# Optimization experiments

Measured on AMD Instinct MI355X. Metric: run time of the kernel, lower is better.

Reference implementation:

```python
import jax, jax.numpy as jnp
import numpy as np

P, LMAX, D, H = 4096, 64, 512, 512
NEG = -1e30


def setup_inputs() -> dict:
    key = jax.random.key(0)
    ks = jax.random.split(key, 8)
    paths_nodes = jax.random.normal(ks[0], (P, LMAX, D), dtype=jnp.float32)
    lengths = jax.random.randint(ks[1], (P,), 1, LMAX + 1, dtype=jnp.int32)
    s = 0.05
    return {
        "paths_nodes": paths_nodes,
        "lengths": lengths,
        "pW1": jax.random.normal(ks[2], (D, H), dtype=jnp.float32) * s,
        "pb1": jnp.zeros((H,), dtype=jnp.float32),
        "pw2": jax.random.normal(ks[3], (H,), dtype=jnp.float32) * s,
        "pb2": jnp.zeros((1,), dtype=jnp.float32),
        "aW1": jax.random.normal(ks[4], (D, H), dtype=jnp.float32) * s,
        "ab1": jnp.zeros((H,), dtype=jnp.float32),
        "aw2": jax.random.normal(ks[5], (H,), dtype=jnp.float32) * s,
        "ab2": jnp.zeros((1,), dtype=jnp.float32),
    }


def reference(paths_nodes, lengths, pW1, pb1, pw2, pb2, aW1, ab1, aw2, ab2):
    # paths_nodes: [P, L, D], lengths: [P]
    mask = jnp.arange(LMAX)[None, :] < lengths[:, None]  # [P, L] valid positions

    # per-path node attention: Linear -> ReLU -> Linear(->1), softmax over length
    h = jax.nn.relu(jnp.einsum('pld,dh->plh', paths_nodes, pW1) + pb1)  # [P,L,H]
    scores = jnp.einsum('plh,h->pl', h, pw2) + pb2[0]                   # [P,L]
    scores = jnp.where(mask, scores, NEG)
    w = jax.nn.softmax(scores, axis=1)                                  # [P,L]
    paths_fea = jnp.einsum('pl,pld->pd', w, paths_nodes)                # [P,D]

    # path-level attention: same MLP over path features, softmax over paths
    h2 = jax.nn.relu(paths_fea @ aW1 + ab1)                             # [P,H]
    a = h2 @ aw2 + ab2[0]                                               # [P]
    aw = jax.nn.softmax(a, axis=0)                                      # [P]
    user_fea = jnp.einsum('p,pd->d', aw, paths_fea)                     # [D]
    return user_fea
```

## Files before the change

kernel.cpp:

```cpp
#include <hip/hip_runtime.h>

typedef __attribute__((ext_vector_type(8))) short bf16x8;
typedef __attribute__((ext_vector_type(8))) unsigned short u16x8;
typedef __attribute__((ext_vector_type(4))) float f32x4;

__device__ __forceinline__ ushort f2bf(float x) {
  unsigned u = __float_as_uint(x);
  unsigned r = (u + 0x7fffu + ((u >> 16) & 1u)) >> 16;
  return (ushort)r;
}

__global__ void transpose_convert(const float* __restrict__ w1, const float* __restrict__ w2,
                                  ushort* __restrict__ o1, ushort* __restrict__ o2) {
  __shared__ float tile[64][65];
  const float* src = (blockIdx.z == 0) ? w1 : w2;
  ushort* dst = (blockIdx.z == 0) ? o1 : o2;
  const int n0 = blockIdx.x * 64, k0 = blockIdx.y * 64;
  const int tx = threadIdx.x, ty = threadIdx.y;
#pragma unroll
  for (int i = 0; i < 16; ++i) {
    int k = ty + i * 4;
    tile[k][tx] = src[(size_t)(k0 + k) * 512 + n0 + tx];
  }
  __syncthreads();
#pragma unroll
  for (int i = 0; i < 16; ++i) {
    int n = ty + i * 4;
    dst[(size_t)(n0 + n) * 512 + k0 + tx] = f2bf(tile[tx][n]);
  }
}

__launch_bounds__(256, 3)
__global__ void gemm_score(const float* __restrict__ A,
                           const ushort* __restrict__ Bt,
                           const float* __restrict__ bias,
                           const float* __restrict__ wout,
                           float* __restrict__ scores) {
  __shared__ ushort As[128 * 64];
  __shared__ ushort Bs[128 * 64];
  __shared__ float sred[2][128];
  const int tid = threadIdx.x;
  const int wv = tid >> 6, lane = tid & 63;
  const int ln = lane & 15, quad = lane >> 4;
  const int wm = wv & 1, wn = wv >> 1;
  const int m0 = blockIdx.y * 128;
  const int nb = blockIdx.x * 128;

  float bv[4], w2v[4];
#pragma unroll
  for (int ns = 0; ns < 4; ++ns) {
    int n = nb + wn * 64 + ns * 16 + ln;
    bv[ns] = bias[n];
    w2v[ns] = wout[n];
  }

  f32x4 acc[4][4];
  const f32x4 zero = {0.f, 0.f, 0.f, 0.f};
#pragma unroll
  for (int i = 0; i < 4; ++i)
#pragma unroll
    for (int j = 0; j < 4; ++j) acc[i][j] = zero;

  int arow[4], brow[4];
#pragma unroll
  for (int ms = 0; ms < 4; ++ms) arow[ms] = wm * 64 + ms * 16 + ln;
#pragma unroll
  for (int ns = 0; ns < 4; ++ns) brow[ns] = wn * 64 + ns * 16 + ln;

  for (int kc = 0; kc < 8; ++kc) {
    const int kb = kc * 64;
    __syncthreads();
#pragma unroll
    for (int j = 0; j < 4; ++j) {
      int id = j * 256 + tid;
      int row = id >> 3, c = id & 7;
      int cs = (c ^ (row & 7)) * 8;
      const float* srcA = A + (size_t)(m0 + row) * 512 + kb + c * 8;
      float4 v0 = *(const float4*)srcA;
      float4 v1 = *(const float4*)(srcA + 4);
      u16x8 ua = {f2bf(v0.x), f2bf(v0.y), f2bf(v0.z), f2bf(v0.w),
                  f2bf(v1.x), f2bf(v1.y), f2bf(v1.z), f2bf(v1.w)};
      *(u16x8*)(&As[row * 64 + cs]) = ua;
      u16x8 ub = *(const u16x8*)(Bt + (size_t)(nb + row) * 512 + kb + c * 8);
      *(u16x8*)(&Bs[row * 64 + cs]) = ub;
    }
    __syncthreads();
#pragma unroll
    for (int k0 = 0; k0 < 2; ++k0) {
      bf16x8 af[4], bfr[4];
#pragma unroll
      for (int ms = 0; ms < 4; ++ms) {
        int r = arow[ms];
        af[ms] = *(const bf16x8*)(&As[r * 64 + (((quad + k0 * 4) ^ (r & 7)) * 8)]);
      }
#pragma unroll
      for (int ns = 0; ns < 4; ++ns) {
        int r = brow[ns];
        bfr[ns] = *(const bf16x8*)(&Bs[r * 64 + (((quad + k0 * 4) ^ (r & 7)) * 8)]);
      }
#pragma unroll
      for (int ms = 0; ms < 4; ++ms)
#pragma unroll
        for (int ns = 0; ns < 4; ++ns)
          acc[ms][ns] = __builtin_amdgcn_mfma_f32_16x16x32_bf16(af[ms], bfr[ns], acc[ms][ns], 0, 0, 0);
    }
  }

#pragma unroll
  for (int ms = 0; ms < 4; ++ms) {
#pragma unroll
    for (int r = 0; r < 4; ++r) {
      float s = 0.f;
#pragma unroll
      for (int ns = 0; ns < 4; ++ns)
        s += fmaxf(acc[ms][ns][r] + bv[ns], 0.f) * w2v[ns];
      s += __shfl_xor(s, 1);
      s += __shfl_xor(s, 2);
      s += __shfl_xor(s, 4);
      s += __shfl_xor(s, 8);
      if (ln == 0) sred[wn][wm * 64 + ms * 16 + quad * 4 + r] = s;
    }
  }
  __syncthreads();
  if (tid < 128) atomicAdd(&scores[m0 + tid], sred[0][tid] + sred[1][tid]);
}

__global__ void node_softmax(float* __restrict__ s_wl, const int* __restrict__ lengths) {
  const int p = blockIdx.x * 4 + (threadIdx.x >> 6);
  const int l = threadIdx.x & 63;
  float s = s_wl[(size_t)p * 64 + l];
  const int len = lengths[p];
  const bool valid = l < len;
  float sv = valid ? s : -1e30f;
  float mx = sv;
  mx = fmaxf(mx, __shfl_xor(mx, 1));
  mx = fmaxf(mx, __shfl_xor(mx, 2));
  mx = fmaxf(mx, __shfl_xor(mx, 4));
  mx = fmaxf(mx, __shfl_xor(mx, 8));
  mx = fmaxf(mx, __shfl_xor(mx, 16));
  mx = fmaxf(mx, __shfl_xor(mx, 32));
  float e = valid ? __expf(sv - mx) : 0.f;
  float tot = e;
  tot += __shfl_xor(tot, 1);
  tot += __shfl_xor(tot, 2);
  tot += __shfl_xor(tot, 4);
  tot += __shfl_xor(tot, 8);
  tot += __shfl_xor(tot, 16);
  tot += __shfl_xor(tot, 32);
  s_wl[(size_t)p * 64 + l] = e / tot;
}

__global__ void wsum(const float* __restrict__ X, const float* __restrict__ wl,
                     float* __restrict__ fea) {
  __shared__ float w[64];
  const int p = blockIdx.x, tid = threadIdx.x;
  if (tid < 64) w[tid] = wl[(size_t)p * 64 + tid];
  __syncthreads();
  const float* Xp = X + (size_t)p * 32768;
  const int d0 = tid * 4;
  float4 a = {0.f, 0.f, 0.f, 0.f};
#pragma unroll
  for (int l = 0; l < 64; ++l) {
    float4 x = *(const float4*)(Xp + l * 512 + d0);
    a.x = fmaf(w[l], x.x, a.x);
    a.y = fmaf(w[l], x.y, a.y);
    a.z = fmaf(w[l], x.z, a.z);
    a.w = fmaf(w[l], x.w, a.w);
  }
  *(float4*)(fea + (size_t)p * 512 + d0) = a;
}

__global__ void softmax_p(const float* __restrict__ a, float* __restrict__ aw) {
  const int tid = threadIdx.x;
  const int wv = tid >> 6;
  __shared__ float redm[4];
  __shared__ float reds[4];
  float v[16];
#pragma unroll
  for (int i = 0; i < 16; ++i) v[i] = a[i * 256 + tid];
  float mx = v[0];
#pragma unroll
  for (int i = 1; i < 16; ++i) mx = fmaxf(mx, v[i]);
  mx = fmaxf(mx, __shfl_xor(mx, 1));
  mx = fmaxf(mx, __shfl_xor(mx, 2));
  mx = fmaxf(mx, __shfl_xor(mx, 4));
  mx = fmaxf(mx, __shfl_xor(mx, 8));
  mx = fmaxf(mx, __shfl_xor(mx, 16));
  mx = fmaxf(mx, __shfl_xor(mx, 32));
  if ((tid & 63) == 0) redm[wv] = mx;
  __syncthreads();
  mx = fmaxf(fmaxf(redm[0], redm[1]), fmaxf(redm[2], redm[3]));
  float s = 0.f;
#pragma unroll
  for (int i = 0; i < 16; ++i) {
    v[i] = __expf(v[i] - mx);
    s += v[i];
  }
  s += __shfl_xor(s, 1);
  s += __shfl_xor(s, 2);
  s += __shfl_xor(s, 4);
  s += __shfl_xor(s, 8);
  s += __shfl_xor(s, 16);
  s += __shfl_xor(s, 32);
  if ((tid & 63) == 0) reds[wv] = s;
  __syncthreads();
  s = reds[0] + reds[1] + reds[2] + reds[3];
  const float inv = 1.f / s;
#pragma unroll
  for (int i = 0; i < 16; ++i) aw[i * 256 + tid] = v[i] * inv;
}

__global__ void user_accum(const float* __restrict__ fea, const float* __restrict__ aw,
                           float* __restrict__ out) {
  const int g = blockIdx.x, tid = threadIdx.x;
  const int d0 = tid * 2;
  float ax = 0.f, ay = 0.f;
  for (int p = g * 64; p < g * 64 + 64; ++p) {
    float w = aw[p];
    float2 x = *(const float2*)(fea + (size_t)p * 512 + d0);
    ax = fmaf(w, x.x, ax);
    ay = fmaf(w, x.y, ay);
  }
  atomicAdd(out + d0, ax);
  atomicAdd(out + d0 + 1, ay);
}

extern "C" void kernel_launch(void* const* d_in, const int* in_sizes, int n_in,
                              void* d_out, int out_size, void* d_ws, size_t ws_size,
                              hipStream_t stream) {
  const float* paths   = (const float*)d_in[0];
  const int*   lengths = (const int*)d_in[1];
  const float* pW1     = (const float*)d_in[2];
  const float* pb1     = (const float*)d_in[3];
  const float* pw2     = (const float*)d_in[4];
  const float* aW1     = (const float*)d_in[6];
  const float* ab1     = (const float*)d_in[7];
  const float* aw2     = (const float*)d_in[8];
  float* out = (float*)d_out;

  char* ws = (char*)d_ws;
  ushort* W1T  = (ushort*)ws;
  ushort* aW1T = (ushort*)(ws + 524288);
  float* nsc   = (float*)(ws + 1048576);
  float* fea   = (float*)(ws + 2097152);
  float* psc   = (float*)(ws + 10485760);
  float* awp   = (float*)(ws + 10502144);

  hipMemsetAsync(nsc, 0, 262144 * sizeof(float), stream);
  hipMemsetAsync(psc, 0, 4096 * sizeof(float), stream);
  hipMemsetAsync(d_out, 0, 512 * sizeof(float), stream);

  transpose_convert<<<dim3(8, 8, 2), dim3(64, 4), 0, stream>>>(pW1, aW1, W1T, aW1T);
  gemm_score<<<dim3(4, 2048), 256, 0, stream>>>(paths, W1T, pb1, pw2, nsc);
  node_softmax<<<1024, 256, 0, stream>>>(nsc, lengths);
  wsum<<<4096, 128, 0, stream>>>(paths, nsc, fea);
  gemm_score<<<dim3(4, 32), 256, 0, stream>>>(fea, aW1T, ab1, aw2, psc);
  softmax_p<<<1, 256, 0, stream>>>(psc, awp);
  user_accum<<<64, 256, 0, stream>>>(fea, awp, out);
}
```

Measured before the change: 985.9 us.

## Pre-convert valid path rows to bf16, skip padded rows in GEMM and weighted sum

```diff
diff --git a/kernel.cpp b/kernel.cpp
--- a/kernel.cpp
+++ b/kernel.cpp
@@ -8,6 +8,12 @@
   unsigned u = __float_as_uint(x);
   unsigned r = (u + 0x7fffu + ((u >> 16) & 1u)) >> 16;
   return (ushort)r;
+}
+
+typedef const __attribute__((address_space(1))) unsigned int ga_uint;
+typedef __attribute__((address_space(3))) unsigned int lds_uint;
+__device__ __forceinline__ void gload_lds16(const ushort* g, ushort* l) {
+  __builtin_amdgcn_global_load_lds((ga_uint*)g, (lds_uint*)l, 16, 0, 0);
 }
 
 __global__ void transpose_convert(const float* __restrict__ w1, const float* __restrict__ w2,
@@ -30,12 +36,120 @@
   }
 }
 
+__global__ void convert_x(const float* __restrict__ X, const int* __restrict__ lengths,
+                          ushort* __restrict__ Y) {
+  const int stride = gridDim.x * blockDim.x;
+  for (int i = blockIdx.x * blockDim.x + threadIdx.x; i < 16777216; i += stride) {
+    const int row = i >> 6;
+    const int l = row & 63, p = row >> 6;
+    if (l < lengths[p]) {
+      const float* s = X + (size_t)i * 8;
+      float4 v0 = *(const float4*)s;
+      float4 v1 = *(const float4*)(s + 4);
+      u16x8 o = {f2bf(v0.x), f2bf(v0.y), f2bf(v0.z), f2bf(v0.w),
+                 f2bf(v1.x), f2bf(v1.y), f2bf(v1.z), f2bf(v1.w)};
+      *(u16x8*)(Y + (size_t)i * 8) = o;
+    }
+  }
+}
+
 __launch_bounds__(256, 3)
-__global__ void gemm_score(const float* __restrict__ A,
-                           const ushort* __restrict__ Bt,
-                           const float* __restrict__ bias,
-                           const float* __restrict__ wout,
-                           float* __restrict__ scores) {
+__global__ void gemm_score_bf16(const ushort* __restrict__ A,
+                                const ushort* __restrict__ Bt,
+                                const float* __restrict__ bias,
+                                const float* __restrict__ wout,
+                                const int* __restrict__ lengths,
+                                float* __restrict__ scores) {
+  __shared__ ushort As[128 * 64] __attribute__((aligned(16)));
+  __shared__ ushort Bs[128 * 64] __attribute__((aligned(16)));
+  __shared__ float sred[2][128];
+  const int tid = threadIdx.x;
+  const int wv = tid >> 6, lane = tid & 63;
+  const int ln = lane & 15, quad = lane >> 4;
+  const int wm = wv & 1, wn = wv >> 1;
+  const int m0 = blockIdx.y * 128;
+  const int nb = blockIdx.x * 128;
+  const int p0 = m0 >> 6;
+
+  const int len0 = lengths[p0], len1 = lengths[p0 + 1];
+  const int mylen = wm ? len1 : len0;
+  const int nms = (mylen + 15) >> 4;
+
+  float bv[4], w2v[4];
+#pragma unroll
+  for (int ns = 0; ns < 4; ++ns) {
+    int n = nb + wn * 64 + ns * 16 + ln;
+    bv[ns] = bias[n];
+    w2v[ns] = wout[n];
+  }
+
+  f32x4 acc[4][4];
+  const f32x4 zero = {0.f, 0.f, 0.f, 0.f};
+#pragma unroll
+  for (int i = 0; i < 4; ++i)
+#pragma unroll
+    for (int j = 0; j < 4; ++j) acc[i][j] = zero;
+
+  for (int kc = 0; kc < 8; ++kc) {
+    const int kb = kc * 64;
+    __syncthreads();
+#pragma unroll
+    for (int i = 0; i < 4; ++i) {
+      const int id = i * 256 + tid;
+      const int row = id >> 3, c = id & 7;
+      const int base = (i * 256 + (tid & ~63)) * 8;
+      const int r0 = i * 32 + wv * 8;
+      const int rlen = (r0 < 64) ? len0 : len1;
+      if ((r0 & 63) < rlen)
+        gload_lds16(A + (size_t)(m0 + row) * 512 + kb + c * 8, &As[base]);
+      gload_lds16(Bt + (size_t)(nb + row) * 512 + kb + c * 8, &Bs[base]);
+    }
+    __syncthreads();
+#pragma unroll
+    for (int k0 = 0; k0 < 2; ++k0) {
+      bf16x8 bfr[4];
+#pragma unroll
+      for (int ns = 0; ns < 4; ++ns)
+        bfr[ns] = *(const bf16x8*)(&Bs[(wn * 64 + ns * 16 + ln) * 64 + (quad + k0 * 4) * 8]);
+#pragma unroll
+      for (int ms = 0; ms < 4; ++ms) {
+        if (ms < nms) {
+          bf16x8 af = *(const bf16x8*)(&As[(wm * 64 + ms * 16 + ln) * 64 + (quad + k0 * 4) * 8]);
+#pragma unroll
+          for (int ns = 0; ns < 4; ++ns)
+            acc[ms][ns] = __builtin_amdgcn_mfma_f32_16x16x32_bf16(af, bfr[ns], acc[ms][ns], 0, 0, 0);
+        }
+      }
+    }
+  }
+
+#pragma unroll
+  for (int ms = 0; ms < 4; ++ms) {
+#pragma unroll
+    for (int r = 0; r < 4; ++r) {
+      float s = 0.f;
+      if (ms < nms) {
+#pragma unroll
+        for (int ns = 0; ns < 4; ++ns)
+          s += fmaxf(acc[ms][ns][r] + bv[ns], 0.f) * w2v[ns];
+        s += __shfl_xor(s, 1);
+        s += __shfl_xor(s, 2);
+        s += __shfl_xor(s, 4);
+        s += __shfl_xor(s, 8);
+      }
+      if (ln == 0) sred[wn][wm * 64 + ms * 16 + quad * 4 + r] = s;
+    }
+  }
+  __syncthreads();
+  if (tid < 128) atomicAdd(&scores[m0 + tid], sred[0][tid] + sred[1][tid]);
+}
+
+__launch_bounds__(256, 3)
+__global__ void gemm_score_f32(const float* __restrict__ A,
+                               const ushort* __restrict__ Bt,
+                               const float* __restrict__ bias,
+                               const float* __restrict__ wout,
+                               float* __restrict__ scores) {
   __shared__ ushort As[128 * 64];
   __shared__ ushort Bs[128 * 64];
   __shared__ float sred[2][128];
@@ -151,16 +265,16 @@
 }
 
 __global__ void wsum(const float* __restrict__ X, const float* __restrict__ wl,
-                     float* __restrict__ fea) {
+                     const int* __restrict__ lengths, float* __restrict__ fea) {
   __shared__ float w[64];
   const int p = blockIdx.x, tid = threadIdx.x;
   if (tid < 64) w[tid] = wl[(size_t)p * 64 + tid];
   __syncthreads();
+  const int len = lengths[p];
   const float* Xp = X + (size_t)p * 32768;
   const int d0 = tid * 4;
   float4 a = {0.f, 0.f, 0.f, 0.f};
-#pragma unroll
-  for (int l = 0; l < 64; ++l) {
+  for (int l = 0; l < len; ++l) {
     float4 x = *(const float4*)(Xp + l * 512 + d0);
     a.x = fmaf(w[l], x.x, a.x);
     a.y = fmaf(w[l], x.y, a.y);
@@ -245,16 +359,23 @@
   float* fea   = (float*)(ws + 2097152);
   float* psc   = (float*)(ws + 10485760);
   float* awp   = (float*)(ws + 10502144);
+  ushort* Xbf  = (ushort*)(ws + 16777216);
+  const bool bf16_path = ws_size >= (16777216ull + 268435456ull);
 
   hipMemsetAsync(nsc, 0, 262144 * sizeof(float), stream);
   hipMemsetAsync(psc, 0, 4096 * sizeof(float), stream);
   hipMemsetAsync(d_out, 0, 512 * sizeof(float), stream);
 
   transpose_convert<<<dim3(8, 8, 2), dim3(64, 4), 0, stream>>>(pW1, aW1, W1T, aW1T);
-  gemm_score<<<dim3(4, 2048), 256, 0, stream>>>(paths, W1T, pb1, pw2, nsc);
+  if (bf16_path) {
+    convert_x<<<2048, 256, 0, stream>>>(paths, lengths, Xbf);
+    gemm_score_bf16<<<dim3(4, 2048), 256, 0, stream>>>(Xbf, W1T, pb1, pw2, lengths, nsc);
+  } else {
+    gemm_score_f32<<<dim3(4, 2048), 256, 0, stream>>>(paths, W1T, pb1, pw2, nsc);
+  }
   node_softmax<<<1024, 256, 0, stream>>>(nsc, lengths);
-  wsum<<<4096, 128, 0, stream>>>(paths, nsc, fea);
-  gemm_score<<<dim3(4, 32), 256, 0, stream>>>(fea, aW1T, ab1, aw2, psc);
+  wsum<<<4096, 128, 0, stream>>>(paths, nsc, lengths, fea);
+  gemm_score_f32<<<dim3(4, 32), 256, 0, stream>>>(fea, aW1T, ab1, aw2, psc);
   softmax_p<<<1, 256, 0, stream>>>(psc, awp);
   user_accum<<<64, 256, 0, stream>>>(fea, awp, out);
 }
```

After: 947.9 us. 3.9% less time.
